# Optimization experiments

Measured on AMD Instinct MI355X. Metric: run time of the kernel, lower is better.

## Reference

```python
import jax, jax.numpy as jnp
import numpy as np

EPS = 1e-5

def inorm(x, w, b):
    # InstanceNorm1d over token dim (axis=1), per (batch, feature); biased var
    m = x.mean(axis=1, keepdims=True)
    v = ((x - m) ** 2).mean(axis=1, keepdims=True)
    return (x - m) / jnp.sqrt(v + EPS) * w + b

def setup_inputs() -> dict:
    B, N, D, FH = 2, 512, 128, 512
    key = jax.random.key(0)
    ks = iter(jax.random.split(key, 48))
    rn = lambda shape, s=0.05: jax.random.normal(next(ks), shape, jnp.float32) * s
    inp = {
        'row_emb': jax.random.normal(next(ks), (B, N, D), jnp.float32),
        'col_emb': jax.random.normal(next(ks), (B, N, D), jnp.float32),
        'cost_mat': jax.random.uniform(next(ks), (B, N, N), jnp.float32),
        'coords': jax.random.uniform(next(ks), (B, N, 2), jnp.float32),
        'alpha': jnp.ones((1,), jnp.float32),
        # instance norm affine params (weight~1, bias~0)
        'n1_w': 1.0 + rn((D,)), 'n1_b': rn((D,)),
        'n2_w': 1.0 + rn((D,)), 'n2_b': rn((D,)),
        'n3_w': 1.0 + rn((D,)), 'n3_b': rn((D,)),
        'fn1_w': 1.0 + rn((D,)), 'fn1_b': rn((D,)),
        'fn2_w': 1.0 + rn((D,)), 'fn2_b': rn((D,)),
        # AFTFull projections (stored (in,out))
        'q_w': rn((D, D)), 'q_b': rn((D,)),
        'k_w': rn((D, D)), 'k_b': rn((D,)),
        'v_w': rn((D, D)), 'v_b': rn((D,)),
        'p_w': rn((D, D)), 'p_b': rn((D,)),
        'mhc_w': rn((D, D)), 'mhc_b': rn((D,)),
        # DistAngleFusion MLPs
        'dist_w1': rn((1, D)), 'dist_b1': rn((D,)),
        'dist_w2': rn((D, D)), 'dist_b2': rn((D,)),
        'ang_w1': rn((1, D)), 'ang_b1': rn((D,)),
        'ang_w2': rn((D, D)), 'ang_b2': rn((D,)),
        'gate_w': rn((2 * D, 1)), 'gate_b': rn((1,)),
        'outlin_w': rn((D, 1)), 'outlin_b': rn((1,)),
        # FeedForward
        'ffn_w1': rn((D, FH)), 'ffn_b1': rn((FH,)),
        'ffn_w2': rn((FH, D)), 'ffn_b2': rn((D,)),
    }
    return inp

def reference(row_emb, col_emb, cost_mat, coords, alpha,
              n1_w, n1_b, n2_w, n2_b, n3_w, n3_b, fn1_w, fn1_b, fn2_w, fn2_b,
              q_w, q_b, k_w, k_b, v_w, v_b, p_w, p_b, mhc_w, mhc_b,
              dist_w1, dist_b1, dist_w2, dist_b2,
              ang_w1, ang_b1, ang_w2, ang_b2,
              gate_w, gate_b, outlin_w, outlin_b,
              ffn_w1, ffn_b1, ffn_w2, ffn_b2):
    rn = inorm(row_emb, n1_w, n1_b)
    cn = inorm(col_emb, n2_w, n2_b)

    # DistAngleFusion: adapt_bias (B,N,N)
    diff = coords[:, :, None, :] - coords[:, None, :, :]  # (B,N,N,2)
    angles = jnp.arctan2(diff[..., 1], diff[..., 0])
    dist_e = jax.nn.relu(cost_mat[..., None] @ dist_w1 + dist_b1) @ dist_w2 + dist_b2  # (B,N,N,D)
    angle_e = jax.nn.relu(angles[..., None] @ ang_w1 + ang_b1) @ ang_w2 + ang_b2
    g = jax.nn.sigmoid(jnp.concatenate([dist_e, angle_e], axis=-1) @ gate_w + gate_b)  # (B,N,N,1)
    fused = g * dist_e + (1.0 - g) * angle_e
    adapt_bias = (fused @ outlin_w + outlin_b)[..., 0] * alpha  # (B,N,N)

    # AFTFull
    Q = jax.nn.sigmoid(rn @ q_w + q_b)          # (B,N,H)
    K = jax.nn.softmax(cn @ k_w + k_b, axis=1)  # softmax over tokens
    V = cn @ v_w + v_b
    eab = jnp.exp(jax.nn.softmax(adapt_bias, axis=-1))  # (B,N,N)
    eK = jnp.exp(K)
    num = jnp.einsum('bnm,bmh->bnh', eab, eK * V)
    den = jnp.einsum('bnm,bmh->bnh', eab, eK)
    Yt = (Q * (num / den)) @ p_w + p_b

    mh = inorm(Yt @ mhc_w + mhc_b, n3_w, n3_b)

    # TransformerFFN with instance norms
    x = inorm(rn + mh, fn1_w, fn1_b)
    ff = jax.nn.relu(x @ ffn_w1 + ffn_b1) @ ffn_w2 + ffn_b2
    return inorm(x + ff, fn2_w, fn2_b)
```

## Files before the change

### kernel.cpp

```cpp
#include <hip/hip_runtime.h>
#include <hip/hip_bf16.h>
#include <math.h>

#define Bn  2
#define Nn  512
#define Dn  128
#define FHn 512

#define PI_F 3.14159265358979323846f

typedef __hip_bfloat16 bf16;

__device__ __forceinline__ float cvt(float x) { return x; }
__device__ __forceinline__ float cvt(bf16 x) { return __bfloat162float(x); }
__device__ __forceinline__ float sigmoidf_(float x) { return 1.0f / (1.0f + __expf(-x)); }
__device__ __forceinline__ bool is_bf16(const void* alpha) {
    return ((const unsigned short*)alpha)[0] == 0x3F80;
}

__device__ __forceinline__ float fatan2f(float dy, float dx) {
    float ax = fabsf(dx), ay = fabsf(dy);
    float mx = fmaxf(ax, ay), mn = fminf(ax, ay);
    float r = __fdividef(mn, mx);
    float t = r * r;
    float a = r * (0.99997726f + t * (-0.33262347f + t * (0.19354346f +
              t * (-0.11643287f + t * (0.05265332f + t * (-0.01172120f))))));
    if (ay > ax) a = 1.57079632679489662f - a;
    if (dx < 0.f) a = PI_F - a;
    if (dy < 0.f) a = -a;
    return fminf(fmaxf(a, -PI_F), PI_F);
}

#define S_ 131072
#define WS_Q    (0 * S_)
#define WS_K    (1 * S_)
#define WS_V    (2 * S_)
#define WS_EK   (3 * S_)
#define WS_EKV  (4 * S_)
#define WS_MH   (5 * S_)
#define WS_T    (6 * S_)
#define WS_OP   (7 * S_)
#define WS_ST   (8 * S_)

#define ST_IN_SC   0
#define ST_IN_SH   512
#define ST_X_SC    2048
#define ST_X_SH    2304
#define ST_PRE     3072
#define P_SC       1024
#define ST_TAB     4224
#define TAB_ANG 644
#define TAB_N   1288
#define ST_LUTC (ST_TAB + TAB_N)
#define ST_LUTA (ST_LUTC + 257)
#define TABLUT_N (TAB_N + 514)

#define SMEM_FLOATS 2568

struct KP {
    const void *row, *col, *cost, *coords, *alpha;
    const void *n1w, *n1b, *n2w, *n2b, *n3w, *n3b, *f1w, *f1b, *f2w, *f2b;
    const void *qw, *qb, *kw, *kb, *vw, *vb, *pw, *pb, *mw, *mb;
    const void *dw1, *db1, *dw2, *db2, *aw1, *ab1, *aw2, *ab2, *gw, *gb, *ow, *ob;
    const void *ffw1, *ffb1, *ffw2, *ffb2;
    void* out;
    float* ws;
};

__device__ __forceinline__ void blk_sum2(float& s, float& ss, volatile float* scr) {
#pragma unroll
    for (int off = 32; off > 0; off >>= 1) { s += __shfl_down(s, off); ss += __shfl_down(ss, off); }
    __syncthreads();
    int wave = threadIdx.x >> 6, lane = threadIdx.x & 63;
    if (lane == 0) { scr[wave] = s; scr[4 + wave] = ss; }
    __syncthreads();
    s = scr[0] + scr[1] + scr[2] + scr[3];
    ss = scr[4] + scr[5] + scr[6] + scr[7];
}

__device__ __forceinline__ float blk_sum1(float v, volatile float* scr) {
#pragma unroll
    for (int off = 32; off > 0; off >>= 1) v += __shfl_down(v, off);
    __syncthreads();
    int wave = threadIdx.x >> 6, lane = threadIdx.x & 63;
    if (lane == 0) scr[wave] = v;
    __syncthreads();
    return scr[0] + scr[1] + scr[2] + scr[3];
}

__device__ __forceinline__ float blk_max1(float v, volatile float* scr) {
#pragma unroll
    for (int off = 32; off > 0; off >>= 1) v = fmaxf(v, __shfl_down(v, off));
    __syncthreads();
    int wave = threadIdx.x >> 6, lane = threadIdx.x & 63;
    if (lane == 0) scr[wave] = v;
    __syncthreads();
    return fmaxf(fmaxf(scr[0], scr[1]), fmaxf(scr[2], scr[3]));
}

template <typename T>
__device__ void build_tables(const T* w1p, const T* b1p, const T* w2p,
                             const T* owp, const T* gwp, float* gtab, float* smem) {
    int tid = threadIdx.x;
    float* W  = smem;
    float* Bb = smem + 128;
    float* U  = smem + 256;
    float* Vv = smem + 384;
    float* Tt = smem + 512;
    int* RK   = (int*)(smem + 640);
    float* STl = smem + 768;
    if (tid < 128) {
        float u = 0.f, v = 0.f;
#pragma unroll 4
        for (int d = 0; d < Dn; ++d) {
            float w2 = cvt(w2p[tid * Dn + d]);
            u += w2 * cvt(owp[d]);
            v += w2 * cvt(gwp[d]);
        }
        float w = cvt(w1p[tid]), b = cvt(b1p[tid]);
        U[tid] = u; Vv[tid] = v; W[tid] = w; Bb[tid] = b;
        Tt[tid] = (w != 0.f) ? (-b / w) : 3.0e38f;
    }
    __syncthreads();
    if (tid < 128) {
        float tk = Tt[tid]; int r = 0;
        for (int j = 0; j < 128; ++j) {
            float tj = Tt[j];
            r += (tj < tk) || (tj == tk && j < tid);
        }
        RK[tid] = r;
        gtab[r] = tk;
        STl[r] = tk;
    }
    __syncthreads();
    if (tid <= 128) {
        int si = tid;
        float slS = 0, inS = 0, slT = 0, inT = 0;
        for (int k = 0; k < 128; ++k) {
            float w = W[k];
            if (w == 0.f) {
                float rb = fmaxf(Bb[k], 0.f);
                inS += rb * U[k];
                inT += rb * Vv[k];
            } else {
                bool act = (w > 0.f) ? (RK[k] < si) : (RK[k] >= si);
                if (act) {
                    slS += w * U[k];  inS += Bb[k] * U[k];
                    slT += w * Vv[k]; inT += Bb[k] * Vv[k];
                }
            }
        }
        gtab[128 + si] = slS;
        gtab[257 + si] = inS;
        gtab[386 + si] = slT;
        gtab[515 + si] = inT;
    }
}

__device__ __forceinline__ int bsearch128(const float* T, float c) {
    int lo = 0, hi = 128;
    while (lo < hi) { int mid = (lo + hi) >> 1; if (T[mid] <= c) lo = mid + 1; else hi = mid; }
    return lo;
}

template <typename T>
__device__ void phase0(const KP& p, float* st, float* smem) {
    float* scr = smem + 2560;
    int cid = blockIdx.x;
    int tid = threadIdx.x;
    {
        int which = cid >> 8, b = (cid >> 7) & 1, d = cid & 127;
        const T* src = (const T*)(which ? p.col : p.row) + (size_t)b * Nn * Dn + d;
        float x0 = cvt(src[(size_t)tid * Dn]);
        float x1 = cvt(src[(size_t)(tid + 256) * Dn]);
        float s = x0 + x1, ss = x0 * x0 + x1 * x1;
        blk_sum2(s, ss, scr);
        if (tid == 0) {
            float m = s * (1.f / Nn);
            float v = fmaxf(ss * (1.f / Nn) - m * m, 0.f);
            float rstd = rsqrtf(v + 1e-5f);
            const T* w = which ? (const T*)p.n2w : (const T*)p.n1w;
            const T* bb = which ? (const T*)p.n2b : (const T*)p.n1b;
            float sc = rstd * cvt(w[d]);
            st[ST_IN_SC + cid] = sc;
            st[ST_IN_SH + cid] = cvt(bb[d]) - m * sc;
        }
    }
    __syncthreads();
    if (cid == 128) {
        const T* db2 = (const T*)p.db2; const T* ab2 = (const T*)p.ab2;
        const T* ow = (const T*)p.ow;   const T* gw = (const T*)p.gw;
        float d2 = 0.f, a2 = 0.f, o = 0.f, g0 = 0.f, g1 = 0.f;
        if (tid < 128) {
            d2 = cvt(db2[tid]); a2 = cvt(ab2[tid]);
            o = cvt(ow[tid]); g0 = cvt(gw[tid]); g1 = cvt(gw[Dn + tid]);
        }
        float cds = d2 * o, cdt = d2 * g0, cas = a2 * o, cat = a2 * g1;
        blk_sum2(cds, cdt, scr);
        blk_sum2(cas, cat, scr);
        if (tid == 0) {
            float* pre = st + ST_PRE;
            pre[P_SC + 0] = cds; pre[P_SC + 1] = cdt;
            pre[P_SC + 2] = cas; pre[P_SC + 3] = cat;
            pre[P_SC + 4] = cvt(((const T*)p.gb)[0]);
            pre[P_SC + 5] = cvt(((const T*)p.ob)[0]);
            pre[P_SC + 6] = cvt(((const T*)p.alpha)[0]);
        }
    } else if (cid == 129) {
        build_tables<T>((const T*)p.dw1, (const T*)p.db1, (const T*)p.dw2,
                        (const T*)p.ow, (const T*)p.gw, st + ST_TAB, smem);
        __syncthreads();
        const float* STl = smem + 768;
        for (int e = tid; e < 257; e += 256) {
            float c = e * (1.f / 256.f);
            st[ST_LUTC + e] = (float)bsearch128(STl, c);
        }
    } else if (cid == 130) {
        build_tables<T>((const T*)p.aw1, (const T*)p.ab1, (const T*)p.aw2,
                        (const T*)p.ow, (const T*)p.gw + Dn, st + ST_TAB + TAB_ANG, smem);
        __syncthreads();
        const float* STl = smem + 768;
        for (int e = tid; e < 257; e += 256) {
            float a = -PI_F + e * (PI_F / 128.f);
            st[ST_LUTA + e] = (float)bsearch128(STl, a);
        }
    }
}

template <typename T>
__device__ void phase1(const KP& p, float* st, float* smem) {
    int tid = threadIdx.x;
    int r0 = blockIdx.x * 4;
    int b = r0 >> 9;
    const T* row = (const T*)p.row; const T* col = (const T*)p.col;
    float* ws = p.ws;
    float* Q = ws + WS_Q; float* Kraw = ws + WS_K; float* V = ws + WS_V;

    float* lr = smem;
    float* lc = smem + 512;
    float* redq = smem + 1024;
    float* redk = smem + 3072;
    float* redv = smem + 5120;
    {
        int r = tid >> 7, d = tid & 127;
        float scR = st[ST_IN_SC + b * 128 + d],       shR = st[ST_IN_SH + b * 128 + d];
        float scC = st[ST_IN_SC + 256 + b * 128 + d], shC = st[ST_IN_SH + 256 + b * 128 + d];
        lr[r * 128 + d] = cvt(row[(size_t)(r0 + r) * Dn + d]) * scR + shR;
        lc[r * 128 + d] = cvt(col[(size_t)(r0 + r) * Dn + d]) * scC + shC;
    }
    __syncthreads();
    {
        int h = tid & 127, q = tid >> 7;
        const T* qw = (const T*)p.qw; const T* kw = (const T*)p.kw; const T* vw = (const T*)p.vw;
        float aq[4] = {0,0,0,0}, ak[4] = {0,0,0,0}, av[4] = {0,0,0,0};
        int ks = q * 32;
#pragma unroll 8
        for (int k = ks; k < ks + 32; ++k) {
            float wq = cvt(qw[k * Dn + h]);
            float wk = cvt(kw[k * Dn + h]);
            float wv = cvt(vw[k * Dn + h]);
#pragma unroll
            for (int r = 0; r < 4; ++r) {
                aq[r] += lr[r * 128 + k] * wq;
                ak[r] += lc[r * 128 + k] * wk;
                av[r] += lc[r * 128 + k] * wv;
            }
        }
#pragma unroll
        for (int r = 0; r < 4; ++r) {
            redq[q * 512 + r * 128 + h] = aq[r];
            redk[q * 512 + r * 128 + h] = ak[r];
            redv[q * 512 + r * 128 + h] = av[r];
        }
    }
    __syncthreads();
    if (tid < 128) {
        int h = tid;
        float bq = cvt(((const T*)p.qb)[h]);
        float bk = cvt(((const T*)p.kb)[h]);
        float bv = cvt(((const T*)p.vb)[h]);
#pragma unroll
        for (int r = 0; r < 4; ++r) {
            float qv = redq[r*128+h] + redq[512 + r*128+h] + redq[1024 + r*128+h] + redq[1536 + r*128+h] + bq;
            float kv = redk[r*128+h] + redk[512 + r*128+h] + redk[1024 + r*128+h] + redk[1536 + r*128+h] + bk;
            float vv = redv[r*128+h] + redv[512 + r*128+h] + redv[1024 + r*128+h] + redv[1536 + r*128+h] + bv;
            Q[(r0 + r) * Dn + h]    = sigmoidf_(qv);
            Kraw[(r0 + r) * Dn + h] = kv;
            V[(r0 + r) * Dn + h]    = vv;
        }
    }
}

__device__ void phase2(const KP& p, float* smem) {
    float* scr = smem + 2560;
    int tid = threadIdx.x;
    int c = blockIdx.x;
    int b = c >> 7, h = c & 127;
    float* ws = p.ws;
    const float* Kraw = ws + WS_K;
    const float* V = ws + WS_V;
    float* eK = ws + WS_EK;
    float* eKV = ws + WS_EKV;
    const float* kb = Kraw + (size_t)b * Nn * Dn + h;
    const float* vb = V + (size_t)b * Nn * Dn + h;
    float x0 = kb[(size_t)tid * Dn];
    float x1 = kb[(size_t)(tid + 256) * Dn];
    float mx = blk_max1(fmaxf(x0, x1), scr);
    float e0 = __expf(x0 - mx), e1 = __expf(x1 - mx);
    float s = blk_sum1(e0 + e1, scr);
    float rs = 1.f / s;
    size_t a0 = (size_t)b * Nn * Dn + (size_t)tid * Dn + h;
    size_t a1 = (size_t)b * Nn * Dn + (size_t)(tid + 256) * Dn + h;
    float ek0 = __expf(e0 * rs), ek1 = __expf(e1 * rs);
    eK[a0] = ek0;  eKV[a0] = ek0 * vb[(size_t)tid * Dn];
    eK[a1] = ek1;  eKV[a1] = ek1 * vb[(size_t)(tid + 256) * Dn];
}

template <typename T>
__device__ void phase3(const KP& p, float* st, float* smem) {
    int tid = threadIdx.x;
    int r0 = blockIdx.x * 4;
    int b = r0 >> 9;
    float* ws = p.ws;
    const float* eK = ws + WS_EK;
    const float* eKV = ws + WS_EKV;
    const float* Q = ws + WS_Q;
    float* mh = ws + WS_MH;

    float* ab   = smem;
    float* redn = smem + 2048;
    float* redd = smem + 4096;
    float* gl   = smem + 6144;
    float* yl   = smem + 6656;
    float* scr  = smem + 7168;

    {
        float* tab  = smem + 2048;
        float* lutc = smem + 3336;
        float* luta = smem + 3593;
        const float* gt = st + ST_TAB;
        for (int e = tid; e < TABLUT_N; e += 512) tab[e] = gt[e];
        __syncthreads();
        const float* pre = st + ST_PRE;
        float cds = pre[P_SC + 0], cdt = pre[P_SC + 1], cas = pre[P_SC + 2], cat = pre[P_SC + 3];
        float gbias = pre[P_SC + 4], obias = pre[P_SC + 5], alpha = pre[P_SC + 6];
        const T* cost = (const T*)p.cost;
        const T* coords = (const T*)p.coords;
        const float* tabA = tab + TAB_ANG;

        int j = tid;
        float cjx = cvt(coords[((size_t)b * Nn + j) * 2 + 0]);
        float cjy = cvt(coords[((size_t)b * Nn + j) * 2 + 1]);
        float av[4];
#pragma unroll
        for (int rr = 0; rr < 4; ++rr) {
            int i = (r0 + rr) & 511;
            float cix = cvt(coords[((size_t)b * Nn + i) * 2 + 0]);
            float ciy = cvt(coords[((size_t)b * Nn + i) * 2 + 1]);
            float c = cvt(cost[(size_t)b * Nn * Nn + (size_t)i * Nn + j]);
            int k = (int)(c * 256.f); k = k < 0 ? 0 : (k > 255 ? 255 : k);
            int lo = (int)lutc[k], hi = (int)lutc[k + 1];
            while (lo < hi && tab[lo] <= c) ++lo;
            float sd = fmaf(tab[128 + lo], c, tab[257 + lo]) + cds;
            float td = fmaf(tab[386 + lo], c, tab[515 + lo]) + cdt;
            float dx = cix - cjx;
            float dy = ciy - cjy;
            float ang = (dx == 0.f && dy == 0.f) ? 0.f : fatan2f(dy, dx);
            int ka = (int)((ang + PI_F) * (128.f / PI_F)); ka = ka < 0 ? 0 : (ka > 255 ? 255 : ka);
            int la = (int)luta[ka], ha = (int)luta[ka + 1];
            while (la < ha && tabA[la] <= ang) ++la;
            float sa = fmaf(tabA[128 + la], ang, tabA[257 + la]) + cas;
            float ta = fmaf(tabA[386 + la], ang, tabA[515 + la]) + cat;
            float gv = sigmoidf_(td + ta + gbias);
            av[rr] = alpha * (gv * sd + (1.f - gv) * sa + obias);
        }
        int wave = tid >> 6, lane = tid & 63;
        float t0 = av[0], t1 = av[1], t2 = av[2], t3 = av[3];
#pragma unroll
        for (int off = 32; off > 0; off >>= 1) {
            t0 = fmaxf(t0, __shfl_down(t0, off));
            t1 = fmaxf(t1, __shfl_down(t1, off));
            t2 = fmaxf(t2, __shfl_down(t2, off));
            t3 = fmaxf(t3, __shfl_down(t3, off));
        }
        __syncthreads();
        if (lane == 0) { scr[wave] = t0; scr[8 + wave] = t1; scr[16 + wave] = t2; scr[24 + wave] = t3; }
        __syncthreads();
        float ev[4];
#pragma unroll
        for (int rr = 0; rr < 4; ++rr) {
            float m = scr[rr * 8];
#pragma unroll
            for (int w = 1; w < 8; ++w) m = fmaxf(m, scr[rr * 8 + w]);
            ev[rr] = __expf(av[rr] - m);
        }
        float s0 = ev[0], s1 = ev[1], s2 = ev[2], s3 = ev[3];
#pragma unroll
        for (int off = 32; off > 0; off >>= 1) {
            s0 += __shfl_down(s0, off);
            s1 += __shfl_down(s1, off);
            s2 += __shfl_down(s2, off);
            s3 += __shfl_down(s3, off);
        }
        if (lane == 0) { scr[32 + wave] = s0; scr[40 + wave] = s1; scr[48 + wave] = s2; scr[56 + wave] = s3; }
        __syncthreads();
#pragma unroll
        for (int rr = 0; rr < 4; ++rr) {
            float s = 0.f;
#pragma unroll
            for (int w = 0; w < 8; ++w) s += scr[32 + rr * 8 + w];
            ab[rr * 512 + j] = __expf(ev[rr] / s);
        }
    }
    __syncthreads();

    int h = tid & 127, q = tid >> 7;
    int j0 = q * 128;

    {
        const float* ekb = eK + (size_t)b * Nn * Dn + h;
        const float* evb = eKV + (size_t)b * Nn * Dn + h;
        float num[4] = {0,0,0,0}, den[4] = {0,0,0,0};
#pragma unroll 4
        for (int j = j0; j < j0 + 128; ++j) {
            float ek = ekb[(size_t)j * Dn];
            float ev_ = evb[(size_t)j * Dn];
#pragma unroll
            for (int r = 0; r < 4; ++r) {
                num[r] += ab[r * 512 + j] * ev_;
                den[r] += ab[r * 512 + j] * ek;
            }
        }
#pragma unroll
        for (int r = 0; r < 4; ++r) {
            redn[q * 512 + r * 128 + h] = num[r];
            redd[q * 512 + r * 128 + h] = den[r];
        }
    }
    __syncthreads();
    if (tid < 128) {
#pragma unroll
        for (int r = 0; r < 4; ++r) {
            float nu = redn[r * 128 + h] + redn[512 + r * 128 + h]
                     + redn[1024 + r * 128 + h] + redn[1536 + r * 128 + h];
            float de = redd[r * 128 + h] + redd[512 + r * 128 + h]
                     + redd[1024 + r * 128 + h] + redd[1536 + r * 128 + h];
            gl[r * 128 + h] = Q[(r0 + r) * Dn + h] * nu / de;
        }
    }
    __syncthreads();
    {
        const T* pw = (const T*)p.pw;
        float acc[4] = {0,0,0,0};
        int ks = q * 32;
#pragma unroll 8
        for (int k = ks; k < ks + 32; ++k) {
            float w = cvt(pw[k * Dn + h]);
#pragma unroll
            for (int r = 0; r < 4; ++r) acc[r] += gl[r * 128 + k] * w;
        }
#pragma unroll
        for (int r = 0; r < 4; ++r) redn[q * 512 + r * 128 + h] = acc[r];
    }
    __syncthreads();
    if (tid < 128) {
        float bp = cvt(((const T*)p.pb)[h]);
#pragma unroll
        for (int r = 0; r < 4; ++r)
            yl[r * 128 + h] = redn[r * 128 + h] + redn[512 + r * 128 + h]
                            + redn[1024 + r * 128 + h] + redn[1536 + r * 128 + h] + bp;
    }
    __syncthreads();
    {
        const T* mw = (const T*)p.mw;
        float acc[4] = {0,0,0,0};
        int ks = q * 32;
#pragma unroll 8
        for (int k = ks; k < ks + 32; ++k) {
            float w = cvt(mw[k * Dn + h]);
#pragma unroll
            for (int r = 0; r < 4; ++r) acc[r] += yl[r * 128 + k] * w;
        }
#pragma unroll
        for (int r = 0; r < 4; ++r) redn[q * 512 + r * 128 + h] = acc[r];
    }
    __syncthreads();
    if (tid < 128) {
        float bm = cvt(((const T*)p.mb)[h]);
#pragma unroll
        for (int r = 0; r < 4; ++r)
            mh[(r0 + r) * Dn + h] = redn[r * 128 + h] + redn[512 + r * 128 + h]
                                  + redn[1024 + r * 128 + h] + redn[1536 + r * 128 + h] + bm;
    }
}

template <typename T>
__device__ void phase45(const KP& p, float* st, float* smem) {
    float* scr = smem + 2560;
    int tid = threadIdx.x;
    int c = blockIdx.x;
    int b = c >> 7, d = c & 127;
    const float* mh = p.ws + WS_MH;
    const float* mp = mh + (size_t)b * Nn * Dn + d;
    float m0 = mp[(size_t)tid * Dn], m1 = mp[(size_t)(tid + 256) * Dn];
    float s = m0 + m1, ss = m0 * m0 + m1 * m1;
    blk_sum2(s, ss, scr);
    float mm = s * (1.f / Nn);
    float vv = fmaxf(ss * (1.f / Nn) - mm * mm, 0.f);
    float rstd = rsqrtf(vv + 1e-5f);
    float scM = rstd * cvt(((const T*)p.n3w)[d]);
    float shM = cvt(((const T*)p.n3b)[d]) - mm * scM;
    const T* row = (const T*)p.row;
    float scI = st[ST_IN_SC + c], shI = st[ST_IN_SH + c];
    const T* rp = row + (size_t)b * Nn * Dn + d;
    float* tp = p.ws + WS_T + (size_t)b * Nn * Dn + d;
    float x0 = cvt(rp[(size_t)tid * Dn]) * scI + shI + m0 * scM + shM;
    float x1 = cvt(rp[(size_t)(tid + 256) * Dn]) * scI + shI + m1 * scM + shM;
    tp[(size_t)tid * Dn] = x0;
    tp[(size_t)(tid + 256) * Dn] = x1;
    __syncthreads();
    float s2 = x0 + x1, ss2 = x0 * x0 + x1 * x1;
    blk_sum2(s2, ss2, scr);
    if (tid == 0) {
        float m = s2 * (1.f / Nn);
        float v = fmaxf(ss2 * (1.f / Nn) - m * m, 0.f);
        float r = rsqrtf(v + 1e-5f);
        float sc = r * cvt(((const T*)p.f1w)[d]);
        st[ST_X_SC + c] = sc;
        st[ST_X_SH + c] = cvt(((const T*)p.f1b)[d]) - m * sc;
    }
}

template <typename T>
__device__ void phase6(const KP& p, float* st, float* smem) {
    int tid = threadIdx.x;
    int r0 = blockIdx.x * 4;
    int b = r0 >> 9;
    const float* t = p.ws + WS_T;
    float* outpre = p.ws + WS_OP;
    const T* w1 = (const T*)p.ffw1; const T* b1 = (const T*)p.ffb1;
    const T* w2 = (const T*)p.ffw2; const T* b2 = (const T*)p.ffb2;

    float* xl = smem;
    float* hl = smem + 512;
    float* red = smem + 2560;
    {
        int r = tid >> 7, d = tid & 127;
        int c = b * 128 + d;
        xl[r * 128 + d] = t[(r0 + r) * Dn + d] * st[ST_X_SC + c] + st[ST_X_SH + c];
    }
    __syncthreads();
    {
        int f = tid;
        float a[4] = {0,0,0,0};
#pragma unroll 4
        for (int k = 0; k < Dn; ++k) {
            float w = cvt(w1[k * FHn + f]);
#pragma unroll
            for (int r = 0; r < 4; ++r) a[r] += xl[r * 128 + k] * w;
        }
        float bb1 = cvt(b1[f]);
#pragma unroll
        for (int r = 0; r < 4; ++r) hl[r * 512 + f] = fmaxf(a[r] + bb1, 0.f);
    }
    __syncthreads();
    {
        int d = tid & 127, q = tid >> 7;
        int k0 = q * 128;
        float a[4] = {0,0,0,0};
#pragma unroll 8
        for (int k = k0; k < k0 + 128; ++k) {
            float w = cvt(w2[k * Dn + d]);
#pragma unroll
            for (int r = 0; r < 4; ++r) a[r] += hl[r * 512 + k] * w;
        }
#pragma unroll
        for (int r = 0; r < 4; ++r) red[q * 512 + r * 128 + d] = a[r];
    }
    __syncthreads();
    if (tid < 128) {
        float bb2 = cvt(b2[tid]);
#pragma unroll
        for (int r = 0; r < 4; ++r) {
            float sum = red[r * 128 + tid] + red[512 + r * 128 + tid]
                      + red[1024 + r * 128 + tid] + red[1536 + r * 128 + tid];
            outpre[(r0 + r) * Dn + tid] = xl[r * 128 + tid] + sum + bb2;
        }
    }
}

template <typename T>
__device__ void phase78(const KP& p, float* smem) {
    float* scr = smem + 2560;
    int tid = threadIdx.x;
    int c = blockIdx.x;
    int b = c >> 7, d = c & 127;
    const float* op = p.ws + WS_OP;
    const float* sp = op + (size_t)b * Nn * Dn + d;
    float x0 = sp[(size_t)tid * Dn], x1 = sp[(size_t)(tid + 256) * Dn];
    float s = x0 + x1, ss = x0 * x0 + x1 * x1;
    blk_sum2(s, ss, scr);
    float m = s * (1.f / Nn);
    float v = fmaxf(ss * (1.f / Nn) - m * m, 0.f);
    float rstd = rsqrtf(v + 1e-5f);
    float sc = rstd * cvt(((const T*)p.f2w)[d]);
    float sh = cvt(((const T*)p.f2b)[d]) - m * sc;
    T* out = (T*)p.out + (size_t)b * Nn * Dn + d;
    out[(size_t)tid * Dn] = (T)(x0 * sc + sh);
    out[(size_t)(tid + 256) * Dn] = (T)(x1 * sc + sh);
}

#define PH_WRAP(name, call_bf, call_f)                                        \
__global__ __launch_bounds__(256) void name(KP p) {                           \
    __shared__ float smem[SMEM_FLOATS];                                       \
    float* st = p.ws + WS_ST; (void)st;                                       \
    if (is_bf16(p.alpha)) { call_bf; } else { call_f; }                       \
}

PH_WRAP(k_head,  phase0<bf16>(p, st, smem),  phase0<float>(p, st, smem))
__global__ __launch_bounds__(512) void k_qkv(KP p) {
    __shared__ float smem[7168];
    float* st = p.ws + WS_ST;
    if (is_bf16(p.alpha)) phase1<bf16>(p, st, smem);
    else                  phase1<float>(p, st, smem);
}
__global__ __launch_bounds__(256) void k_kekv(KP p) {
    __shared__ float smem[SMEM_FLOATS];
    phase2(p, smem);
}
__global__ __launch_bounds__(512) void k_attn(KP p) {
    __shared__ float smem[7232];
    float* st = p.ws + WS_ST;
    if (is_bf16(p.alpha)) phase3<bf16>(p, st, smem);
    else                  phase3<float>(p, st, smem);
}
PH_WRAP(k_mid,   phase45<bf16>(p, st, smem), phase45<float>(p, st, smem))
__global__ __launch_bounds__(512) void k_ffn(KP p) {
    __shared__ float smem[4608];
    float* st = p.ws + WS_ST;
    if (is_bf16(p.alpha)) phase6<bf16>(p, st, smem);
    else                  phase6<float>(p, st, smem);
}
PH_WRAP(k_tail,  phase78<bf16>(p, smem),     phase78<float>(p, smem))

extern "C" void kernel_launch(void* const* d_in, const int* in_sizes, int n_in,
                              void* d_out, int out_size, void* d_ws, size_t ws_size,
                              hipStream_t stream) {
    KP p;
    p.row = d_in[0];  p.col = d_in[1];  p.cost = d_in[2];  p.coords = d_in[3];
    p.alpha = d_in[4];
    p.n1w = d_in[5];  p.n1b = d_in[6];  p.n2w = d_in[7];  p.n2b = d_in[8];
    p.n3w = d_in[9];  p.n3b = d_in[10]; p.f1w = d_in[11]; p.f1b = d_in[12];
    p.f2w = d_in[13]; p.f2b = d_in[14];
    p.qw = d_in[15];  p.qb = d_in[16];  p.kw = d_in[17];  p.kb = d_in[18];
    p.vw = d_in[19];  p.vb = d_in[20];  p.pw = d_in[21];  p.pb = d_in[22];
    p.mw = d_in[23];  p.mb = d_in[24];
    p.dw1 = d_in[25]; p.db1 = d_in[26]; p.dw2 = d_in[27]; p.db2 = d_in[28];
    p.aw1 = d_in[29]; p.ab1 = d_in[30]; p.aw2 = d_in[31]; p.ab2 = d_in[32];
    p.gw = d_in[33];  p.gb = d_in[34];  p.ow = d_in[35];  p.ob = d_in[36];
    p.ffw1 = d_in[37]; p.ffb1 = d_in[38]; p.ffw2 = d_in[39]; p.ffb2 = d_in[40];
    p.out = d_out;
    p.ws = (float*)d_ws;

    k_head<<<512, 256, 0, stream>>>(p);
    k_qkv<<<256, 512, 0, stream>>>(p);
    k_kekv<<<256, 256, 0, stream>>>(p);
    k_attn<<<256, 512, 0, stream>>>(p);
    k_mid<<<256, 256, 0, stream>>>(p);
    k_ffn<<<256, 512, 0, stream>>>(p);
    k_tail<<<256, 256, 0, stream>>>(p);
}
```

Baseline: 231.5 us.

## Double thread counts in norm/softmax and attention kernels, one element per thread

The column-reduction kernels (K softmax, mid instance norms, tail norm) now launch 512 threads so each thread handles one token, and use new 8-wave block reductions with tiny shared scratch. The attention kernel moves to 1024 threads: bias computation splits rows across two halves, the num/den accumulation is split into eight 64-token chunks, and the two projection matvecs become one full 128-long dot per thread instead of partial sums plus a reduction pass. The aim is more parallelism and latency hiding on a grid of only 256 blocks, at the cost of larger shared memory in the attention kernel and longer per-thread serial loops in the projections.

```diff
diff --git a/kernel.cpp b/kernel.cpp
--- a/kernel.cpp
+++ b/kernel.cpp
@@ -78,24 +78,42 @@
     ss = scr[4] + scr[5] + scr[6] + scr[7];
 }
 
-__device__ __forceinline__ float blk_sum1(float v, volatile float* scr) {
+__device__ __forceinline__ void blk512_sum2(float& s, float& ss, volatile float* scr) {
+#pragma unroll
+    for (int off = 32; off > 0; off >>= 1) { s += __shfl_down(s, off); ss += __shfl_down(ss, off); }
+    __syncthreads();
+    int wave = threadIdx.x >> 6, lane = threadIdx.x & 63;
+    if (lane == 0) { scr[wave] = s; scr[8 + wave] = ss; }
+    __syncthreads();
+    s = 0.f; ss = 0.f;
+#pragma unroll
+    for (int w = 0; w < 8; ++w) { s += scr[w]; ss += scr[8 + w]; }
+}
+
+__device__ __forceinline__ float blk512_sum1(float v, volatile float* scr) {
 #pragma unroll
     for (int off = 32; off > 0; off >>= 1) v += __shfl_down(v, off);
     __syncthreads();
     int wave = threadIdx.x >> 6, lane = threadIdx.x & 63;
     if (lane == 0) scr[wave] = v;
     __syncthreads();
-    return scr[0] + scr[1] + scr[2] + scr[3];
-}
-
-__device__ __forceinline__ float blk_max1(float v, volatile float* scr) {
+    float s = 0.f;
+#pragma unroll
+    for (int w = 0; w < 8; ++w) s += scr[w];
+    return s;
+}
+
+__device__ __forceinline__ float blk512_max1(float v, volatile float* scr) {
 #pragma unroll
     for (int off = 32; off > 0; off >>= 1) v = fmaxf(v, __shfl_down(v, off));
     __syncthreads();
     int wave = threadIdx.x >> 6, lane = threadIdx.x & 63;
     if (lane == 0) scr[wave] = v;
     __syncthreads();
-    return fmaxf(fmaxf(scr[0], scr[1]), fmaxf(scr[2], scr[3]));
+    float m = scr[0];
+#pragma unroll
+    for (int w = 1; w < 8; ++w) m = fmaxf(m, scr[w]);
+    return m;
 }
 
 template <typename T>
@@ -292,7 +310,7 @@
 }
 
 __device__ void phase2(const KP& p, float* smem) {
-    float* scr = smem + 2560;
+    float* scr = smem;
     int tid = threadIdx.x;
     int c = blockIdx.x;
     int b = c >> 7, h = c & 127;
@@ -304,16 +322,13 @@
     const float* kb = Kraw + (size_t)b * Nn * Dn + h;
     const float* vb = V + (size_t)b * Nn * Dn + h;
     float x0 = kb[(size_t)tid * Dn];
-    float x1 = kb[(size_t)(tid + 256) * Dn];
-    float mx = blk_max1(fmaxf(x0, x1), scr);
-    float e0 = __expf(x0 - mx), e1 = __expf(x1 - mx);
-    float s = blk_sum1(e0 + e1, scr);
+    float mx = blk512_max1(x0, scr);
+    float e0 = __expf(x0 - mx);
+    float s = blk512_sum1(e0, scr);
     float rs = 1.f / s;
     size_t a0 = (size_t)b * Nn * Dn + (size_t)tid * Dn + h;
-    size_t a1 = (size_t)b * Nn * Dn + (size_t)(tid + 256) * Dn + h;
-    float ek0 = __expf(e0 * rs), ek1 = __expf(e1 * rs);
+    float ek0 = __expf(e0 * rs);
     eK[a0] = ek0;  eKV[a0] = ek0 * vb[(size_t)tid * Dn];
-    eK[a1] = ek1;  eKV[a1] = ek1 * vb[(size_t)(tid + 256) * Dn];
 }
 
 template <typename T>
@@ -329,17 +344,17 @@
 
     float* ab   = smem;
     float* redn = smem + 2048;
-    float* redd = smem + 4096;
-    float* gl   = smem + 6144;
-    float* yl   = smem + 6656;
-    float* scr  = smem + 7168;
+    float* redd = smem + 6144;
+    float* gl   = smem + 10240;
+    float* yl   = smem + 10752;
+    float* scr  = smem + 11264;
 
     {
         float* tab  = smem + 2048;
         float* lutc = smem + 3336;
         float* luta = smem + 3593;
         const float* gt = st + ST_TAB;
-        for (int e = tid; e < TABLUT_N; e += 512) tab[e] = gt[e];
+        for (int e = tid; e < TABLUT_N; e += 1024) tab[e] = gt[e];
         __syncthreads();
         const float* pre = st + ST_PRE;
         float cds = pre[P_SC + 0], cdt = pre[P_SC + 1], cas = pre[P_SC + 2], cat = pre[P_SC + 3];
@@ -348,13 +363,15 @@
         const T* coords = (const T*)p.coords;
         const float* tabA = tab + TAB_ANG;
 
-        int j = tid;
+        int j = tid & 511;
+        int rp = tid >> 9;
         float cjx = cvt(coords[((size_t)b * Nn + j) * 2 + 0]);
         float cjy = cvt(coords[((size_t)b * Nn + j) * 2 + 1]);
-        float av[4];
-#pragma unroll
-        for (int rr = 0; rr < 4; ++rr) {
-            int i = (r0 + rr) & 511;
+        float av[2];
+#pragma unroll
+        for (int rr = 0; rr < 2; ++rr) {
+            int row = rp * 2 + rr;
+            int i = (r0 + row) & 511;
             float cix = cvt(coords[((size_t)b * Nn + i) * 2 + 0]);
             float ciy = cvt(coords[((size_t)b * Nn + i) * 2 + 1]);
             float c = cvt(cost[(size_t)b * Nn * Nn + (size_t)i * Nn + j]);
@@ -374,55 +391,53 @@
             float gv = sigmoidf_(td + ta + gbias);
             av[rr] = alpha * (gv * sd + (1.f - gv) * sa + obias);
         }
-        int wave = tid >> 6, lane = tid & 63;
-        float t0 = av[0], t1 = av[1], t2 = av[2], t3 = av[3];
+        int wave = tid >> 6, lane = tid & 63, w8 = wave & 7;
+        float t0 = av[0], t1 = av[1];
 #pragma unroll
         for (int off = 32; off > 0; off >>= 1) {
             t0 = fmaxf(t0, __shfl_down(t0, off));
             t1 = fmaxf(t1, __shfl_down(t1, off));
-            t2 = fmaxf(t2, __shfl_down(t2, off));
-            t3 = fmaxf(t3, __shfl_down(t3, off));
         }
         __syncthreads();
-        if (lane == 0) { scr[wave] = t0; scr[8 + wave] = t1; scr[16 + wave] = t2; scr[24 + wave] = t3; }
+        if (lane == 0) { scr[(rp * 2) * 8 + w8] = t0; scr[(rp * 2 + 1) * 8 + w8] = t1; }
         __syncthreads();
-        float ev[4];
-#pragma unroll
-        for (int rr = 0; rr < 4; ++rr) {
-            float m = scr[rr * 8];
-#pragma unroll
-            for (int w = 1; w < 8; ++w) m = fmaxf(m, scr[rr * 8 + w]);
+        float ev[2];
+#pragma unroll
+        for (int rr = 0; rr < 2; ++rr) {
+            int row = rp * 2 + rr;
+            float m = scr[row * 8];
+#pragma unroll
+            for (int w = 1; w < 8; ++w) m = fmaxf(m, scr[row * 8 + w]);
             ev[rr] = __expf(av[rr] - m);
         }
-        float s0 = ev[0], s1 = ev[1], s2 = ev[2], s3 = ev[3];
+        float s0 = ev[0], s1 = ev[1];
 #pragma unroll
         for (int off = 32; off > 0; off >>= 1) {
             s0 += __shfl_down(s0, off);
             s1 += __shfl_down(s1, off);
-            s2 += __shfl_down(s2, off);
-            s3 += __shfl_down(s3, off);
-        }
-        if (lane == 0) { scr[32 + wave] = s0; scr[40 + wave] = s1; scr[48 + wave] = s2; scr[56 + wave] = s3; }
+        }
+        if (lane == 0) { scr[32 + (rp * 2) * 8 + w8] = s0; scr[32 + (rp * 2 + 1) * 8 + w8] = s1; }
         __syncthreads();
 #pragma unroll
-        for (int rr = 0; rr < 4; ++rr) {
+        for (int rr = 0; rr < 2; ++rr) {
+            int row = rp * 2 + rr;
             float s = 0.f;
 #pragma unroll
-            for (int w = 0; w < 8; ++w) s += scr[32 + rr * 8 + w];
-            ab[rr * 512 + j] = __expf(ev[rr] / s);
+            for (int w = 0; w < 8; ++w) s += scr[32 + row * 8 + w];
+            ab[row * 512 + j] = __expf(ev[rr] / s);
         }
     }
     __syncthreads();
 
     int h = tid & 127, q = tid >> 7;
-    int j0 = q * 128;
+    int j0 = q * 64;
 
     {
         const float* ekb = eK + (size_t)b * Nn * Dn + h;
         const float* evb = eKV + (size_t)b * Nn * Dn + h;
         float num[4] = {0,0,0,0}, den[4] = {0,0,0,0};
 #pragma unroll 4
-        for (int j = j0; j < j0 + 128; ++j) {
+        for (int j = j0; j < j0 + 64; ++j) {
             float ek = ekb[(size_t)j * Dn];
             float ev_ = evb[(size_t)j * Dn];
 #pragma unroll
@@ -438,73 +453,49 @@
         }
     }
     __syncthreads();
-    if (tid < 128) {
-#pragma unroll
-        for (int r = 0; r < 4; ++r) {
-            float nu = redn[r * 128 + h] + redn[512 + r * 128 + h]
-                     + redn[1024 + r * 128 + h] + redn[1536 + r * 128 + h];
-            float de = redd[r * 128 + h] + redd[512 + r * 128 + h]
-                     + redd[1024 + r * 128 + h] + redd[1536 + r * 128 + h];
-            gl[r * 128 + h] = Q[(r0 + r) * Dn + h] * nu / de;
-        }
-    }
-    __syncthreads();
-    {
+    if (tid < 512) {
+        int r = tid >> 7;
+        float nu = 0.f, de = 0.f;
+#pragma unroll
+        for (int qq = 0; qq < 8; ++qq) {
+            nu += redn[qq * 512 + r * 128 + h];
+            de += redd[qq * 512 + r * 128 + h];
+        }
+        gl[r * 128 + h] = Q[(r0 + r) * Dn + h] * nu / de;
+    }
+    __syncthreads();
+    if (tid < 512) {
+        int r = tid >> 7;
         const T* pw = (const T*)p.pw;
-        float acc[4] = {0,0,0,0};
-        int ks = q * 32;
+        const float* glr = gl + r * 128;
+        float acc = 0.f;
 #pragma unroll 8
-        for (int k = ks; k < ks + 32; ++k) {
-            float w = cvt(pw[k * Dn + h]);
-#pragma unroll
-            for (int r = 0; r < 4; ++r) acc[r] += gl[r * 128 + k] * w;
-        }
-#pragma unroll
-        for (int r = 0; r < 4; ++r) redn[q * 512 + r * 128 + h] = acc[r];
-    }
-    __syncthreads();
-    if (tid < 128) {
-        float bp = cvt(((const T*)p.pb)[h]);
-#pragma unroll
-        for (int r = 0; r < 4; ++r)
-            yl[r * 128 + h] = redn[r * 128 + h] + redn[512 + r * 128 + h]
-                            + redn[1024 + r * 128 + h] + redn[1536 + r * 128 + h] + bp;
-    }
-    __syncthreads();
-    {
+        for (int k = 0; k < 128; ++k) acc += glr[k] * cvt(pw[k * Dn + h]);
+        yl[r * 128 + h] = acc + cvt(((const T*)p.pb)[h]);
+    }
+    __syncthreads();
+    if (tid < 512) {
+        int r = tid >> 7;
         const T* mw = (const T*)p.mw;
-        float acc[4] = {0,0,0,0};
-        int ks = q * 32;
+        const float* ylr = yl + r * 128;
+        float acc = 0.f;
 #pragma unroll 8
-        for (int k = ks; k < ks + 32; ++k) {
-            float w = cvt(mw[k * Dn + h]);
-#pragma unroll
-            for (int r = 0; r < 4; ++r) acc[r] += yl[r * 128 + k] * w;
-        }
-#pragma unroll
-        for (int r = 0; r < 4; ++r) redn[q * 512 + r * 128 + h] = acc[r];
-    }
-    __syncthreads();
-    if (tid < 128) {
-        float bm = cvt(((const T*)p.mb)[h]);
-#pragma unroll
-        for (int r = 0; r < 4; ++r)
-            mh[(r0 + r) * Dn + h] = redn[r * 128 + h] + redn[512 + r * 128 + h]
-                                  + redn[1024 + r * 128 + h] + redn[1536 + r * 128 + h] + bm;
+        for (int k = 0; k < 128; ++k) acc += ylr[k] * cvt(mw[k * Dn + h]);
+        mh[(r0 + r) * Dn + h] = acc + cvt(((const T*)p.mb)[h]);
     }
 }
 
 template <typename T>
 __device__ void phase45(const KP& p, float* st, float* smem) {
-    float* scr = smem + 2560;
+    float* scr = smem;
     int tid = threadIdx.x;
     int c = blockIdx.x;
     int b = c >> 7, d = c & 127;
     const float* mh = p.ws + WS_MH;
     const float* mp = mh + (size_t)b * Nn * Dn + d;
-    float m0 = mp[(size_t)tid * Dn], m1 = mp[(size_t)(tid + 256) * Dn];
-    float s = m0 + m1, ss = m0 * m0 + m1 * m1;
-    blk_sum2(s, ss, scr);
+    float m0 = mp[(size_t)tid * Dn];
+    float s = m0, ss = m0 * m0;
+    blk512_sum2(s, ss, scr);
     float mm = s * (1.f / Nn);
     float vv = fmaxf(ss * (1.f / Nn) - mm * mm, 0.f);
     float rstd = rsqrtf(vv + 1e-5f);
@@ -515,12 +506,10 @@
     const T* rp = row + (size_t)b * Nn * Dn + d;
     float* tp = p.ws + WS_T + (size_t)b * Nn * Dn + d;
     float x0 = cvt(rp[(size_t)tid * Dn]) * scI + shI + m0 * scM + shM;
-    float x1 = cvt(rp[(size_t)(tid + 256) * Dn]) * scI + shI + m1 * scM + shM;
     tp[(size_t)tid * Dn] = x0;
-    tp[(size_t)(tid + 256) * Dn] = x1;
-    __syncthreads();
-    float s2 = x0 + x1, ss2 = x0 * x0 + x1 * x1;
-    blk_sum2(s2, ss2, scr);
+    __syncthreads();
+    float s2 = x0, ss2 = x0 * x0;
+    blk512_sum2(s2, ss2, scr);
     if (tid == 0) {
         float m = s2 * (1.f / Nn);
         float v = fmaxf(ss2 * (1.f / Nn) - m * m, 0.f);
@@ -591,15 +580,15 @@
 
 template <typename T>
 __device__ void phase78(const KP& p, float* smem) {
-    float* scr = smem + 2560;
+    float* scr = smem;
     int tid = threadIdx.x;
     int c = blockIdx.x;
     int b = c >> 7, d = c & 127;
     const float* op = p.ws + WS_OP;
     const float* sp = op + (size_t)b * Nn * Dn + d;
-    float x0 = sp[(size_t)tid * Dn], x1 = sp[(size_t)(tid + 256) * Dn];
-    float s = x0 + x1, ss = x0 * x0 + x1 * x1;
-    blk_sum2(s, ss, scr);
+    float x0 = sp[(size_t)tid * Dn];
+    float s = x0, ss = x0 * x0;
+    blk512_sum2(s, ss, scr);
     float m = s * (1.f / Nn);
     float v = fmaxf(ss * (1.f / Nn) - m * m, 0.f);
     float rstd = rsqrtf(v + 1e-5f);
@@ -607,41 +596,47 @@
     float sh = cvt(((const T*)p.f2b)[d]) - m * sc;
     T* out = (T*)p.out + (size_t)b * Nn * Dn + d;
     out[(size_t)tid * Dn] = (T)(x0 * sc + sh);
-    out[(size_t)(tid + 256) * Dn] = (T)(x1 * sc + sh);
-}
-
-#define PH_WRAP(name, call_bf, call_f)                                        \
-__global__ __launch_bounds__(256) void name(KP p) {                           \
-    __shared__ float smem[SMEM_FLOATS];                                       \
-    float* st = p.ws + WS_ST; (void)st;                                       \
-    if (is_bf16(p.alpha)) { call_bf; } else { call_f; }                       \
-}
-
-PH_WRAP(k_head,  phase0<bf16>(p, st, smem),  phase0<float>(p, st, smem))
+}
+
+__global__ __launch_bounds__(256) void k_head(KP p) {
+    __shared__ float smem[SMEM_FLOATS];
+    float* st = p.ws + WS_ST;
+    if (is_bf16(p.alpha)) phase0<bf16>(p, st, smem);
+    else                  phase0<float>(p, st, smem);
+}
 __global__ __launch_bounds__(512) void k_qkv(KP p) {
     __shared__ float smem[7168];
     float* st = p.ws + WS_ST;
     if (is_bf16(p.alpha)) phase1<bf16>(p, st, smem);
     else                  phase1<float>(p, st, smem);
 }
-__global__ __launch_bounds__(256) void k_kekv(KP p) {
-    __shared__ float smem[SMEM_FLOATS];
+__global__ __launch_bounds__(512) void k_kekv(KP p) {
+    __shared__ float smem[16];
     phase2(p, smem);
 }
-__global__ __launch_bounds__(512) void k_attn(KP p) {
-    __shared__ float smem[7232];
+__global__ __launch_bounds__(1024) void k_attn(KP p) {
+    __shared__ float smem[11328];
     float* st = p.ws + WS_ST;
     if (is_bf16(p.alpha)) phase3<bf16>(p, st, smem);
     else                  phase3<float>(p, st, smem);
 }
-PH_WRAP(k_mid,   phase45<bf16>(p, st, smem), phase45<float>(p, st, smem))
+__global__ __launch_bounds__(512) void k_mid(KP p) {
+    __shared__ float smem[16];
+    float* st = p.ws + WS_ST;
+    if (is_bf16(p.alpha)) phase45<bf16>(p, st, smem);
+    else                  phase45<float>(p, st, smem);
+}
 __global__ __launch_bounds__(512) void k_ffn(KP p) {
     __shared__ float smem[4608];
     float* st = p.ws + WS_ST;
     if (is_bf16(p.alpha)) phase6<bf16>(p, st, smem);
     else                  phase6<float>(p, st, smem);
 }
-PH_WRAP(k_tail,  phase78<bf16>(p, smem),     phase78<float>(p, smem))
+__global__ __launch_bounds__(512) void k_tail(KP p) {
+    __shared__ float smem[16];
+    if (is_bf16(p.alpha)) phase78<bf16>(p, smem);
+    else                  phase78<float>(p, smem);
+}
 
 extern "C" void kernel_launch(void* const* d_in, const int* in_sizes, int n_in,
                               void* d_out, int out_size, void* d_ws, size_t ws_size,
@@ -664,9 +659,9 @@
 
     k_head<<<512, 256, 0, stream>>>(p);
     k_qkv<<<256, 512, 0, stream>>>(p);
-    k_kekv<<<256, 256, 0, stream>>>(p);
-    k_attn<<<256, 512, 0, stream>>>(p);
-    k_mid<<<256, 256, 0, stream>>>(p);
+    k_kekv<<<256, 512, 0, stream>>>(p);
+    k_attn<<<256, 1024, 0, stream>>>(p);
+    k_mid<<<256, 512, 0, stream>>>(p);
     k_ffn<<<256, 512, 0, stream>>>(p);
-    k_tail<<<256, 256, 0, stream>>>(p);
-}
+    k_tail<<<256, 512, 0, stream>>>(p);
+}
```

Measured after the change: 230.5 us. Within noise of the previous version (-0.4%).
